# Kernel tuning notes

Hardware: AMD Instinct MI355X
Metric: run time of the kernel (lower is better)

Reference implementation:

```python
import jax, jax.numpy as jnp
import numpy as np

PATCH = 768
POS = 64
HID = 512
B, N = 8, 2048


def setup_inputs() -> dict:
    key = jax.random.key(0)
    ks = jax.random.split(key, 8)
    d_in = PATCH + POS
    s = 1.0 / np.sqrt(d_in)
    return {
        "patches": jax.random.normal(ks[0], (B, N, PATCH), jnp.float32),
        "positions": jax.random.normal(ks[1], (B, N, POS), jnp.float32),
        "Wq": jax.random.uniform(ks[2], (d_in, HID), jnp.float32, -s, s),
        "bq": jax.random.uniform(ks[3], (HID,), jnp.float32, -s, s),
        "Wk": jax.random.uniform(ks[4], (d_in, HID), jnp.float32, -s, s),
        "bk": jax.random.uniform(ks[5], (d_in and HID,), jnp.float32, -s, s),
        "Wv": jax.random.uniform(ks[6], (d_in, HID), jnp.float32, -s, s),
        "bv": jax.random.uniform(ks[7], (HID,), jnp.float32, -s, s),
    }


def reference(patches, positions, Wq, bq, Wk, bk, Wv, bv):
    # concat patch features with positional features: [B, N, PATCH+POS]
    x = jnp.concatenate([patches, positions], axis=-1)
    Q = x @ Wq + bq  # [B, N, HID]
    K = x @ Wk + bk
    V = x @ Wv + bv
    scale = jnp.sqrt(jnp.asarray(HID, x.dtype))
    scores = jnp.einsum("bnd,bmd->bnm", Q, K) / scale  # [B, N, N]
    weights = jax.nn.softmax(scores, axis=-1)
    return jnp.einsum("bnm,bmd->bnd", weights, V)  # [B, N, HID]
```

## Files before the change

kernel.cpp:

```cpp
#include <hip/hip_runtime.h>
#include <hip/hip_bf16.h>
#include <math.h>

typedef __hip_bfloat16 bf16;
typedef __attribute__((ext_vector_type(4))) float f32x4;
typedef __attribute__((ext_vector_type(8))) short s16x8;

typedef const __attribute__((address_space(1))) void gvoid_t;
typedef __attribute__((address_space(3))) void lvoid_t;

__device__ __forceinline__ void gload16(const void* g, void* l) {
  __builtin_amdgcn_global_load_lds((gvoid_t*)g, (lvoid_t*)l, 16, 0, 0);
}
__device__ __forceinline__ unsigned short f2b(float f) {
  bf16 h = __float2bfloat16(f);
  return *(unsigned short*)&h;
}

__global__ __launch_bounds__(256) void prep_x(const float* __restrict__ patches,
                                              const float* __restrict__ positions,
                                              bf16* __restrict__ xb) {
  const int c = threadIdx.x;
  const bool lo = (c < 192);
  const bool hi = (c >= 192) && (c < 208);
  if (!(lo || hi)) return;
  const int dst = lo ? (c * 4) : (768 + (c - 192) * 4);
  #pragma unroll
  for (int rr = 0; rr < 8; ++rr) {
    const long long row = (long long)blockIdx.x * 8 + rr;
    const float* src = lo ? (patches + row * 768 + c * 4)
                          : (positions + row * 64 + (c - 192) * 4);
    float4 v = *(const float4*)src;
    uint2 w;
    w.x = (unsigned int)f2b(v.x) | ((unsigned int)f2b(v.y) << 16);
    w.y = (unsigned int)f2b(v.z) | ((unsigned int)f2b(v.w) << 16);
    *(uint2*)(xb + row * 832 + dst) = w;
  }
}

__global__ __launch_bounds__(256) void prep_w(const float* __restrict__ Wq,
                                              const float* __restrict__ Wk,
                                              const float* __restrict__ Wv,
                                              bf16* __restrict__ Wt) {
  __shared__ float tile[32][33];
  const int z = blockIdx.z;
  const float* W = (z == 0) ? Wq : (z == 1) ? Wk : Wv;
  bf16* T = Wt + (long long)z * 512 * 832;
  const int n0 = blockIdx.x * 32;
  const int k0 = blockIdx.y * 32;
  const int tx = threadIdx.x, ty = threadIdx.y;
  #pragma unroll
  for (int i = 0; i < 32; i += 8)
    tile[ty + i][tx] = W[(long long)(k0 + ty + i) * 512 + n0 + tx];
  __syncthreads();
  #pragma unroll
  for (int i = 0; i < 32; i += 8)
    T[(long long)(n0 + ty + i) * 832 + k0 + tx] = __float2bfloat16(tile[tx][ty + i]);
}

#define VMW5  asm volatile("s_waitcnt vmcnt(5)" ::: "memory")
#define VMW8  asm volatile("s_waitcnt vmcnt(8)" ::: "memory")
#define VMW10 asm volatile("s_waitcnt vmcnt(10)" ::: "memory")
#define PBAR __builtin_amdgcn_s_barrier()

__device__ __forceinline__ void stage_half(const bf16* src, char* lds, int stride) {
  gload16(src, lds);
  gload16(src + 64 * stride, lds + 8192);
}
__device__ __forceinline__ void stage_b192(const bf16* src, char* lds) {
  gload16(src, lds);
  gload16(src + 64 * 832, lds + 8192);
  gload16(src + 128 * 832, lds + 16384);
}
__device__ __forceinline__ void lda4(const bf16* base, int rowbase, int llo,
                                     int xk0, int xk1, s16x8 af[4][2]) {
  #pragma unroll
  for (int mf = 0; mf < 4; mf++) {
    const bf16* p = base + (rowbase + mf * 16 + llo) * 64;
    af[mf][0] = *(const s16x8*)(p + xk0);
    af[mf][1] = *(const s16x8*)(p + xk1);
  }
}
__device__ __forceinline__ void ldb2(const bf16* base, int rowbase, int llo,
                                     int xk0, int xk1, s16x8 bfr[2][2]) {
  #pragma unroll
  for (int nf = 0; nf < 2; nf++) {
    const bf16* p = base + (rowbase + nf * 16 + llo) * 64;
    bfr[nf][0] = *(const s16x8*)(p + xk0);
    bfr[nf][1] = *(const s16x8*)(p + xk1);
  }
}
__device__ __forceinline__ void ldb3(const bf16* base, int rowbase, int llo,
                                     int xk0, int xk1, s16x8 bfr[3][2]) {
  #pragma unroll
  for (int nf = 0; nf < 3; nf++) {
    const bf16* p = base + (rowbase + nf * 16 + llo) * 64;
    bfr[nf][0] = *(const s16x8*)(p + xk0);
    bfr[nf][1] = *(const s16x8*)(p + xk1);
  }
}
__device__ __forceinline__ void mma16(f32x4 acc[4][2], s16x8 af[4][2],
                                      s16x8 bfr[2][2]) {
  __builtin_amdgcn_s_setprio(1);
  #pragma unroll
  for (int mf = 0; mf < 4; mf++)
    #pragma unroll
    for (int nf = 0; nf < 2; nf++) {
      acc[mf][nf] = __builtin_amdgcn_mfma_f32_16x16x32_bf16(
          af[mf][0], bfr[nf][0], acc[mf][nf], 0, 0, 0);
      acc[mf][nf] = __builtin_amdgcn_mfma_f32_16x16x32_bf16(
          af[mf][1], bfr[nf][1], acc[mf][nf], 0, 0, 0);
    }
  __builtin_amdgcn_s_setprio(0);
}
__device__ __forceinline__ void mma24(f32x4 acc[4][3], s16x8 af[4][2],
                                      s16x8 bfr[3][2]) {
  __builtin_amdgcn_s_setprio(1);
  #pragma unroll
  for (int mf = 0; mf < 4; mf++)
    #pragma unroll
    for (int nf = 0; nf < 3; nf++) {
      acc[mf][nf] = __builtin_amdgcn_mfma_f32_16x16x32_bf16(
          af[mf][0], bfr[nf][0], acc[mf][nf], 0, 0, 0);
      acc[mf][nf] = __builtin_amdgcn_mfma_f32_16x16x32_bf16(
          af[mf][1], bfr[nf][1], acc[mf][nf], 0, 0, 0);
    }
  __builtin_amdgcn_s_setprio(0);
}

#define QKV_TILE(abuf, bbuf, bstage, ka1, kb2)                               \
  do {                                                                       \
                                                               \
    lda4(As2[abuf], wm * 64, llo, xk0, xk1, af);                             \
    ldb3(Bs3[bbuf], wn * 48, llo, xk0, xk1, bfr);                            \
    stage_half(sA + (ka1), (char*)As2[(abuf) ^ 1] + wofs, 832);              \
    stage_b192(sB + (kb2), (char*)Bs3[bstage] + wofs);                       \
    VMW5; PBAR;                                                              \
    mma24(acc[0], af, bfr);                                                  \
                               \
    lda4(As2[abuf], 128 + wm * 64, llo, xk0, xk1, af);                       \
    stage_half(sA + 128 * 832 + (ka1), (char*)As2[(abuf) ^ 1] + 16384 + wofs,\
               832);                                                         \
    VMW5; PBAR;                                                              \
    mma24(acc[1], af, bfr);                                                  \
  } while (0)

__global__ __launch_bounds__(512, 2) void gemm_qkv(
    const bf16* __restrict__ xb, const bf16* __restrict__ Wt,
    const float* __restrict__ bq, const float* __restrict__ bk,
    const float* __restrict__ bv,
    bf16* __restrict__ qk, bf16* __restrict__ vt) {
  __shared__ bf16 As2[2][256 * 64];
  __shared__ bf16 Bs3[3][192 * 64];
  const int tid = threadIdx.x;
  const int wave = tid >> 6, lane = tid & 63;
  const int llo = lane & 15, lhi = lane >> 4;
  const int wm = wave >> 2, wn = wave & 3;

  const unsigned int lin = blockIdx.x;
  const unsigned int xcd = lin & 7u, idx = lin >> 3;
  const unsigned int g = xcd * 64u + idx;
  const int bm_t = (int)(g >> 3);
  const int bn_t = (int)(g & 7u);
  const int row0 = bm_t * 256;
  const int col0 = bn_t * 192;

  const int sr = tid >> 3;
  const int kkofs = ((tid & 7) ^ (sr & 7)) << 3;
  const bf16* sA = xb + (long long)(row0 + sr) * 832 + kkofs;
  const bf16* sB = Wt + (long long)(col0 + sr) * 832 + kkofs;
  const int wofs = wave * 1024;

  const int xk0 = ((lhi ^ (llo & 7)) << 3);
  const int xk1 = (((4 + lhi) ^ (llo & 7)) << 3);

  f32x4 acc[2][4][3] = {};
  s16x8 af[4][2], bfr[3][2];

  stage_half(sA, (char*)As2[0] + wofs, 832);
  stage_b192(sB, (char*)Bs3[0] + wofs);
  stage_half(sA + 128 * 832, (char*)As2[0] + 16384 + wofs, 832);
  stage_b192(sB + 64, (char*)Bs3[1] + wofs);
  VMW5; PBAR;

  for (int jj = 0; jj < 2; ++jj) {
    const int u0 = jj * 6;
    QKV_TILE(0, 0, 2, (u0 + 1) * 64, (u0 + 2) * 64);
    QKV_TILE(1, 1, 0, (u0 + 2) * 64, (u0 + 3) * 64);
    QKV_TILE(0, 2, 1, (u0 + 3) * 64, (u0 + 4) * 64);
    QKV_TILE(1, 0, 2, (u0 + 4) * 64, (u0 + 5) * 64);
    QKV_TILE(0, 1, 0, (u0 + 5) * 64, (u0 + 6) * 64);
    QKV_TILE(1, 2, 1, (u0 + 6) * 64, ((u0 + 7) <= 12 ? (u0 + 7) * 64 : 768));
  }
  QKV_TILE(0, 0, 2, 768, 768);

  asm volatile("s_waitcnt vmcnt(0)" ::: "memory");

  #pragma unroll
  for (int qr = 0; qr < 2; qr++)
    #pragma unroll
    for (int mf = 0; mf < 4; mf++)
      #pragma unroll
      for (int nf = 0; nf < 3; nf++) {
        const int c = col0 + wn * 48 + nf * 16 + llo;
        const int z = c >> 9, cc = c & 511;
        const int grow0 = row0 + qr * 128 + wm * 64 + mf * 16 + lhi * 4;
        if (z < 2) {
          const float bb = (z ? bk : bq)[cc];
          bf16* outp = qk + (long long)z * 16384 * 512;
          #pragma unroll
          for (int r = 0; r < 4; r++)
            outp[(long long)(grow0 + r) * 512 + cc] =
                __float2bfloat16(acc[qr][mf][nf][r] + bb);
        } else {
          const int b = grow0 >> 11, j = grow0 & 2047;
          const float bb = bv[cc];
          uint2 w;
          w.x = (unsigned int)f2b(acc[qr][mf][nf][0] + bb) |
                ((unsigned int)f2b(acc[qr][mf][nf][1] + bb) << 16);
          w.y = (unsigned int)f2b(acc[qr][mf][nf][2] + bb) |
                ((unsigned int)f2b(acc[qr][mf][nf][3] + bb) << 16);
          *(uint2*)(vt + (long long)b * 512 * 2048 + (long long)cc * 2048 + j) = w;
        }
      }
}
#undef QKV_TILE

__global__ __launch_bounds__(512, 2) void gemm_scores(const bf16* __restrict__ qk,
                                                      bf16* __restrict__ S,
                                                      float* __restrict__ rowsumP) {
  __shared__ bf16 As[2][256 * 64];
  __shared__ bf16 Bs[2][256 * 64];
  const int tid = threadIdx.x;
  const int wave = tid >> 6, lane = tid & 63;
  const int llo = lane & 15, lhi = lane >> 4;
  const int wm = wave >> 2, wn = wave & 3;

  const unsigned int lin = blockIdx.x;
  const int b = (int)(lin & 7u);
  const unsigned int idx = lin >> 3;
  const int row0 = (int)(idx >> 3) * 256;
  const int coltile = (int)(idx & 7u);
  const int col0 = coltile * 256;

  const bf16* Ab = qk + (long long)b * 2048 * 512;
  const bf16* Bb = qk + (long long)16384 * 512 + (long long)b * 2048 * 512;

  const int sr = tid >> 3;
  const int kkofs = ((tid & 7) ^ (sr & 7)) << 3;
  const bf16* sA = Ab + (long long)(row0 + sr) * 512 + kkofs;
  const bf16* sB = Bb + (long long)(col0 + sr) * 512 + kkofs;
  const int wofs = wave * 1024;

  const int xk0 = ((lhi ^ (llo & 7)) << 3);
  const int xk1 = (((4 + lhi) ^ (llo & 7)) << 3);

  f32x4 acc[2][2][4][2] = {};
  s16x8 af[4][2], bf0[2][2], bf1[2][2];

  stage_half(sA, (char*)As[0] + wofs, 512);
  stage_half(sB, (char*)Bs[0] + wofs, 512);
  stage_half(sB + 128 * 512, (char*)Bs[0] + 16384 + wofs, 512);
  stage_half(sA + 128 * 512, (char*)As[0] + 16384 + wofs, 512);
  stage_half(sA + 64, (char*)As[1] + wofs, 512);
  stage_half(sB + 64, (char*)Bs[1] + wofs, 512);
  VMW8; PBAR;

  for (int i = 0; i < 4; ++i) {
    const int kt1 = (2 * i + 1) * 64;
    const int kt2 = (2 * i + 2 < 8) ? (2 * i + 2) * 64 : 448;
    const int kt3 = (2 * i + 3 < 8) ? (2 * i + 3) * 64 : 448;
    lda4(As[0], wm * 64, llo, xk0, xk1, af);
    ldb2(Bs[0], wn * 32, llo, xk0, xk1, bf0);
    stage_half(sB + 128 * 512 + kt1, (char*)Bs[1] + 16384 + wofs, 512);
    VMW8; PBAR;
    mma16(acc[0][0], af, bf0);
    ldb2(Bs[0], 128 + wn * 32, llo, xk0, xk1, bf1);
    stage_half(sA + 128 * 512 + kt1, (char*)As[1] + 16384 + wofs, 512);
    VMW8; PBAR;
    mma16(acc[0][1], af, bf1);
    lda4(As[0], 128 + wm * 64, llo, xk0, xk1, af);
    stage_half(sA + kt2, (char*)As[0] + wofs, 512);
    PBAR;
    mma16(acc[1][0], af, bf0);
    stage_half(sB + kt2, (char*)Bs[0] + wofs, 512);
    VMW8; PBAR;
    mma16(acc[1][1], af, bf1);
    lda4(As[1], wm * 64, llo, xk0, xk1, af);
    ldb2(Bs[1], wn * 32, llo, xk0, xk1, bf0);
    stage_half(sB + 128 * 512 + kt2, (char*)Bs[0] + 16384 + wofs, 512);
    VMW8; PBAR;
    mma16(acc[0][0], af, bf0);
    ldb2(Bs[1], 128 + wn * 32, llo, xk0, xk1, bf1);
    stage_half(sA + 128 * 512 + kt2, (char*)As[0] + 16384 + wofs, 512);
    VMW8; PBAR;
    mma16(acc[0][1], af, bf1);
    lda4(As[1], 128 + wm * 64, llo, xk0, xk1, af);
    stage_half(sA + kt3, (char*)As[1] + wofs, 512);
    PBAR;
    mma16(acc[1][0], af, bf0);
    stage_half(sB + kt3, (char*)Bs[1] + wofs, 512);
    VMW8; PBAR;
    mma16(acc[1][1], af, bf1);
  }

  __syncthreads();

  const float alpha = 0.044194173824159216f;
  bf16* Sb = S + (long long)b * 2048 * 2048;
  #pragma unroll
  for (int qr = 0; qr < 2; qr++)
    #pragma unroll
    for (int qc = 0; qc < 2; qc++)
      #pragma unroll
      for (int mf = 0; mf < 4; mf++)
        #pragma unroll
        for (int nf = 0; nf < 2; nf++) {
          #pragma unroll
          for (int r = 0; r < 4; r++)
            acc[qr][qc][mf][nf][r] = __expf(acc[qr][qc][mf][nf][r] * alpha);
          const int gcol = col0 + qc * 128 + wn * 32 + nf * 16 + llo;
          const int grow0 = row0 + qr * 128 + wm * 64 + mf * 16 + lhi * 4;
          #pragma unroll
          for (int r = 0; r < 4; r++)
            Sb[(long long)(grow0 + r) * 2048 + gcol] =
                __float2bfloat16(acc[qr][qc][mf][nf][r]);
        }

  float* psum = (float*)As;
  #pragma unroll
  for (int qr = 0; qr < 2; qr++)
    #pragma unroll
    for (int mf = 0; mf < 4; mf++)
      #pragma unroll
      for (int r = 0; r < 4; r++) {
        float p = acc[qr][0][mf][0][r] + acc[qr][0][mf][1][r] +
                  acc[qr][1][mf][0][r] + acc[qr][1][mf][1][r];
        p += __shfl_xor(p, 1, 64);
        p += __shfl_xor(p, 2, 64);
        p += __shfl_xor(p, 4, 64);
        p += __shfl_xor(p, 8, 64);
        if (llo == 0)
          psum[wn * 256 + qr * 128 + wm * 64 + mf * 16 + lhi * 4 + r] = p;
      }
  __syncthreads();
  if (tid < 256) {
    const float v = psum[tid] + psum[256 + tid] + psum[512 + tid] + psum[768 + tid];
    rowsumP[(long long)(b * 8 + coltile) * 2048 + row0 + tid] = v;
  }
}

#define PV_TILE(c, cs, kstage)                                              \
  do {                                                                      \
                                                              \
    lda4(As3[c], wm * 64, llo, xk0, xk1, af);                               \
    ldb2(Bs3[c], wn * 32, llo, xk0, xk1, bfr);                              \
    stage_half(sA + (kstage), (char*)As3[cs] + wofs, 2048);                 \
    stage_half(sB + (kstage), (char*)Bs3[cs] + wofs, 2048);                 \
    VMW10; PBAR;                                                            \
    mma16(acc[0], af, bfr);                                                 \
                              \
    lda4(As3[c], 128 + wm * 64, llo, xk0, xk1, af);                         \
    stage_half(sA + 128 * 2048 + (kstage), (char*)As3[cs] + 16384 + wofs,   \
               2048);                                                      \
    VMW8; PBAR;                                                             \
    mma16(acc[1], af, bfr);                                                 \
  } while (0)

__global__ __launch_bounds__(512, 2) void gemm_pv(const bf16* __restrict__ S,
                                                  const bf16* __restrict__ vt,
                                                  const float* __restrict__ rowsumP,
                                                  float* __restrict__ out) {
  __shared__ bf16 As3[3][256 * 64];
  __shared__ bf16 Bs3[3][128 * 64];
  const int tid = threadIdx.x;
  const int wave = tid >> 6, lane = tid & 63;
  const int llo = lane & 15, lhi = lane >> 4;
  const int wm = wave >> 2, wn = wave & 3;

  const unsigned int lin = blockIdx.x;
  const int b = (int)(lin & 7u);
  const unsigned int idx = lin >> 3;
  const int row0 = (int)(idx >> 2) * 256;
  const int col0 = (int)(idx & 3u) * 128;

  const bf16* Ab = S + (long long)b * 2048 * 2048;
  const bf16* Bb = vt + (long long)b * 512 * 2048;

  const int sr = tid >> 3;
  const int kkofs = ((tid & 7) ^ (sr & 7)) << 3;
  const bf16* sA = Ab + (long long)(row0 + sr) * 2048 + kkofs;
  const bf16* sB = Bb + (long long)(col0 + sr) * 2048 + kkofs;
  const int wofs = wave * 1024;

  const int xk0 = ((lhi ^ (llo & 7)) << 3);
  const int xk1 = (((4 + lhi) ^ (llo & 7)) << 3);

  f32x4 acc[2][4][2] = {};
  s16x8 af[4][2], bfr[2][2];

  stage_half(sA, (char*)As3[0] + wofs, 2048);
  stage_half(sB, (char*)Bs3[0] + wofs, 2048);
  stage_half(sA + 128 * 2048, (char*)As3[0] + 16384 + wofs, 2048);
  stage_half(sA + 64, (char*)As3[1] + wofs, 2048);
  stage_half(sB + 64, (char*)Bs3[1] + wofs, 2048);
  stage_half(sA + 128 * 2048 + 64, (char*)As3[1] + 16384 + wofs, 2048);
  VMW8; PBAR;

  for (int j = 0; j < 10; ++j) {
    const int kb = j * 192;
    PV_TILE(0, 2, kb + 128);
    PV_TILE(1, 0, kb + 192);
    PV_TILE(2, 1, kb + 256);
  }
  PV_TILE(0, 2, 1984);
  PV_TILE(1, 0, 1984);

  asm volatile("s_waitcnt vmcnt(0)" ::: "memory");
  __syncthreads();

  float* rrow = (float*)As3[1];
  if (tid < 256) {
    const float* rp = rowsumP + ((long long)b * 8) * 2048 + row0 + tid;
    float s = 0.f;
    #pragma unroll
    for (int t = 0; t < 8; t++) s += rp[t * 2048];
    rrow[tid] = 1.0f / s;
  }
  __syncthreads();

  float* Ob = out + (long long)b * 2048 * 512;
  #pragma unroll
  for (int qr = 0; qr < 2; qr++)
    #pragma unroll
    for (int mf = 0; mf < 4; mf++) {
      const int grow0 = row0 + qr * 128 + wm * 64 + mf * 16 + lhi * 4;
      float iv[4];
      #pragma unroll
      for (int r = 0; r < 4; r++) iv[r] = rrow[grow0 - row0 + r];
      #pragma unroll
      for (int nf = 0; nf < 2; nf++) {
        const int gcol = col0 + wn * 32 + nf * 16 + llo;
        #pragma unroll
        for (int r = 0; r < 4; r++)
          Ob[(long long)(grow0 + r) * 512 + gcol] = acc[qr][mf][nf][r] * iv[r];
      }
    }
}
#undef PV_TILE

extern "C" void kernel_launch(void* const* d_in, const int* in_sizes, int n_in,
                              void* d_out, int out_size, void* d_ws, size_t ws_size,
                              hipStream_t stream) {
  const float* patches = (const float*)d_in[0];
  const float* positions = (const float*)d_in[1];
  const float* Wq = (const float*)d_in[2];
  const float* bq = (const float*)d_in[3];
  const float* Wk = (const float*)d_in[4];
  const float* bk = (const float*)d_in[5];
  const float* Wv = (const float*)d_in[6];
  const float* bv = (const float*)d_in[7];
  float* out = (float*)d_out;

  if (ws_size < 149422080u) return;

  char* ws = (char*)d_ws;
  bf16* Wt = (bf16*)(ws);
  bf16* xb = (bf16*)(ws + 2555904);
  bf16* qk = (bf16*)(ws + 29818880);
  bf16* vt = (bf16*)(ws + 63373312);
  bf16* S  = (bf16*)(ws + 80150528);
  float* rowsumP = (float*)(ws + 147324928);

  prep_x<<<2048, 256, 0, stream>>>(patches, positions, xb);
  prep_w<<<dim3(16, 26, 3), dim3(32, 8), 0, stream>>>(Wq, Wk, Wv, Wt);
  gemm_qkv<<<512, 512, 0, stream>>>(xb, Wt, bq, bk, bv, qk, vt);
  gemm_scores<<<512, 512, 0, stream>>>(qk, S, rowsumP);
  gemm_pv<<<256, 512, 0, stream>>>(S, vt, rowsumP, out);
}
```

Before: 258.2 us.

## Restructure QK^T score GEMM prefetch schedule with fewer vmcnt waits

Reorders the global-to-LDS staging in the scores GEMM main loop. Each wave now issues one stage per MMA group, waits on vmcnt only twice per loop iteration instead of six times, and wraps each MMA block in barriers. The prologue also stages the second B half-tile for buffer 1 early. The aim is to cut stalls on outstanding loads and overlap memory with MFMA better, at the cost of extra barriers and the risk of LDS buffer races if the new wait placement is wrong.

After: 256.2 us. No clear change (-0.7%).

```diff
diff --git a/kernel.cpp b/kernel.cpp
--- a/kernel.cpp
+++ b/kernel.cpp
@@ -59,6 +59,7 @@
 }
 
 #define VMW5  asm volatile("s_waitcnt vmcnt(5)" ::: "memory")
+#define VMW6  asm volatile("s_waitcnt vmcnt(6)" ::: "memory")
 #define VMW8  asm volatile("s_waitcnt vmcnt(8)" ::: "memory")
 #define VMW10 asm volatile("s_waitcnt vmcnt(10)" ::: "memory")
 #define PBAR __builtin_amdgcn_s_barrier()
@@ -264,7 +265,8 @@
   stage_half(sA + 128 * 512, (char*)As[0] + 16384 + wofs, 512);
   stage_half(sA + 64, (char*)As[1] + wofs, 512);
   stage_half(sB + 64, (char*)Bs[1] + wofs, 512);
-  VMW8; PBAR;
+  stage_half(sB + 128 * 512 + 64, (char*)Bs[1] + 16384 + wofs, 512);
+  VMW6; PBAR;
 
   for (int i = 0; i < 4; ++i) {
     const int kt1 = (2 * i + 1) * 64;
@@ -272,36 +274,28 @@
     const int kt3 = (2 * i + 3 < 8) ? (2 * i + 3) * 64 : 448;
     lda4(As[0], wm * 64, llo, xk0, xk1, af);
     ldb2(Bs[0], wn * 32, llo, xk0, xk1, bf0);
-    stage_half(sB + 128 * 512 + kt1, (char*)Bs[1] + 16384 + wofs, 512);
-    VMW8; PBAR;
-    mma16(acc[0][0], af, bf0);
+    stage_half(sA + 128 * 512 + kt1, (char*)As[1] + 16384 + wofs, 512);
+    PBAR; mma16(acc[0][0], af, bf0); PBAR;
     ldb2(Bs[0], 128 + wn * 32, llo, xk0, xk1, bf1);
-    stage_half(sA + 128 * 512 + kt1, (char*)As[1] + 16384 + wofs, 512);
-    VMW8; PBAR;
-    mma16(acc[0][1], af, bf1);
+    stage_half(sA + kt2, (char*)As[0] + wofs, 512);
+    PBAR; mma16(acc[0][1], af, bf1); PBAR;
     lda4(As[0], 128 + wm * 64, llo, xk0, xk1, af);
-    stage_half(sA + kt2, (char*)As[0] + wofs, 512);
-    PBAR;
-    mma16(acc[1][0], af, bf0);
     stage_half(sB + kt2, (char*)Bs[0] + wofs, 512);
-    VMW8; PBAR;
-    mma16(acc[1][1], af, bf1);
+    PBAR; mma16(acc[1][0], af, bf0); PBAR;
+    stage_half(sB + 128 * 512 + kt2, (char*)Bs[0] + 16384 + wofs, 512);
+    VMW6; PBAR; mma16(acc[1][1], af, bf1); PBAR;
     lda4(As[1], wm * 64, llo, xk0, xk1, af);
     ldb2(Bs[1], wn * 32, llo, xk0, xk1, bf0);
-    stage_half(sB + 128 * 512 + kt2, (char*)Bs[0] + 16384 + wofs, 512);
-    VMW8; PBAR;
-    mma16(acc[0][0], af, bf0);
+    stage_half(sA + 128 * 512 + kt2, (char*)As[0] + 16384 + wofs, 512);
+    PBAR; mma16(acc[0][0], af, bf0); PBAR;
     ldb2(Bs[1], 128 + wn * 32, llo, xk0, xk1, bf1);
-    stage_half(sA + 128 * 512 + kt2, (char*)As[0] + 16384 + wofs, 512);
-    VMW8; PBAR;
-    mma16(acc[0][1], af, bf1);
+    stage_half(sA + kt3, (char*)As[1] + wofs, 512);
+    PBAR; mma16(acc[0][1], af, bf1); PBAR;
     lda4(As[1], 128 + wm * 64, llo, xk0, xk1, af);
-    stage_half(sA + kt3, (char*)As[1] + wofs, 512);
-    PBAR;
-    mma16(acc[1][0], af, bf0);
     stage_half(sB + kt3, (char*)Bs[1] + wofs, 512);
-    VMW8; PBAR;
-    mma16(acc[1][1], af, bf1);
+    PBAR; mma16(acc[1][0], af, bf0); PBAR;
+    stage_half(sB + 128 * 512 + kt3, (char*)Bs[1] + 16384 + wofs, 512);
+    VMW6; PBAR; mma16(acc[1][1], af, bf1); PBAR;
   }
 
   __syncthreads();
```
